# Optimization experiments

Hardware: AMD Instinct MI355X
Metric: run time of the kernel (lower is better)

Reference implementation:

```python
import jax, jax.numpy as jnp
import numpy as np

N_HEAD = 16

def _proj(W, b, x):
    # 1x1 Conv2d: x is (b, e, h, w) -> (b, o, h, w)
    return jnp.einsum('oe,behw->bohw', W, x) + b[None, :, None, None]

def setup_inputs() -> dict:
    key = jax.random.key(0)
    ks = jax.random.split(key, 12)
    B, E, S = 2, 1024, 2048
    d_qk, d_v, d_out = E, E, E
    def xavier(k, o, i):
        bound = np.sqrt(6.0 / (o + i))
        return jax.random.uniform(k, (o, i), jnp.float32, -bound, bound)
    return {
        'q': jax.random.normal(ks[0], (B, E, 1, S), jnp.float32),
        'k': jax.random.normal(ks[1], (B, E, 1, S), jnp.float32),
        'v': jax.random.normal(ks[2], (B, E, 1, S), jnp.float32),
        'qk_mask': jax.random.normal(ks[3], (B, S, 1, S), jnp.float32),
        'Wq': xavier(ks[4], d_qk, E), 'bq': jnp.zeros((d_qk,), jnp.float32),
        'Wk': xavier(ks[5], d_qk, E), 'bk': jnp.zeros((d_qk,), jnp.float32),
        'Wv': xavier(ks[6], d_v, E), 'bv': jnp.zeros((d_v,), jnp.float32),
        'Wo': xavier(ks[7], d_out, d_v), 'bo': jnp.zeros((d_out,), jnp.float32),
    }

def reference(q, k, v, qk_mask, Wq, bq, Wk, bk, Wv, bv, Wo, bo):
    # q,k,v: (B, E, 1, S); qk_mask: (B, S_src, 1, S_tgt)
    qp = _proj(Wq, bq, q)
    kp = _proj(Wk, bk, k)
    vp = _proj(Wv, bv, v)
    B, C, _, S = qp.shape
    H = N_HEAD
    dh = C // H
    scale = float(dh) ** -0.5
    qh = (qp * scale).reshape(B, H, dh, S)   # (b, h, c, q)
    kh = kp.reshape(B, H, dh, S)             # (b, h, c, k)
    vh = vp.reshape(B, H, dh, S)             # (b, h, c, k)
    # per-head scores, equivalent to the split einsum 'bchq,bkhc->bkhq'
    scores = jnp.einsum('bhcq,bhck->bhkq', qh, kh)        # (b, h, k, q)
    scores = scores + qk_mask[:, None, :, 0, :]           # mask broadcast over heads
    w = jax.nn.softmax(scores, axis=2)                    # softmax over key dim (dim=1 per-head)
    attn = jnp.einsum('bhkq,bhck->bhcq', w, vh).reshape(B, C, 1, S)
    return _proj(Wo, bo, attn)
```

## Files before the change

kernel.cpp:

```cpp
#include <hip/hip_runtime.h>
#include <hip/hip_bf16.h>

typedef unsigned short ushort_t;
typedef __attribute__((ext_vector_type(8))) __bf16 bf16x8;
typedef __attribute__((ext_vector_type(4))) float f32x4;
typedef __attribute__((ext_vector_type(2))) unsigned int u32x2;
typedef __attribute__((ext_vector_type(8))) unsigned short us8;

#define DEV __device__ __forceinline__

constexpr int BB = 2, EE = 1024, SS = 2048, HH = 16;
constexpr float L2E = 1.44269504088896f;
constexpr float SCALE_Q = 0.125f * 1.44269504088896f;

DEV ushort_t f2bf(float x) {
  union { float f; unsigned u; } c; c.f = x;
  unsigned u = c.u;
  return (ushort_t)((u + 0x7fffu + ((u >> 16) & 1u)) >> 16);
}

DEV unsigned cvtpk(float lo, float hi) {
  unsigned r;
  asm volatile("v_cvt_pk_bf16_f32 %0, %1, %2" : "=v"(r) : "v"(lo), "v"(hi));
  return r;
}

DEV void gload16(const void* g, void* l) {
  __builtin_amdgcn_global_load_lds((const __attribute__((address_space(1))) void*)g,
                                   (__attribute__((address_space(3))) void*)l, 16, 0, 0);
}

struct TpArgs { const float* i0; const float* i1; const float* i2;
                ushort_t* o0; ushort_t* o1; ushort_t* o2; };

__global__ __launch_bounds__(256) void k_transpose_cvt(TpArgs a) {
  int z = blockIdx.z; int p = z >> 1; int b = z & 1;
  const float* in = (p == 0) ? a.i0 : (p == 1) ? a.i1 : a.i2;
  ushort_t* out = (p == 0) ? a.o0 : (p == 1) ? a.o1 : a.o2;
  in += (long long)b * EE * SS;
  out += (long long)b * SS * EE;
  int s0 = blockIdx.x * 64, e0 = blockIdx.y * 64;
  __shared__ __align__(16) ushort_t T[64][72];
  int t = threadIdx.x;
  int sc = (t & 15) * 4, erb = t >> 4;
#pragma unroll
  for (int it = 0; it < 4; ++it) {
    int er = erb + it * 16;
    float4 v = *(const float4*)(in + (long long)(e0 + er) * SS + s0 + sc);
    T[sc + 0][er] = f2bf(v.x);
    T[sc + 1][er] = f2bf(v.y);
    T[sc + 2][er] = f2bf(v.z);
    T[sc + 3][er] = f2bf(v.w);
  }
  __syncthreads();
#pragma unroll
  for (int it = 0; it < 2; ++it) {
    int slot = t + it * 256;
    int sr = slot >> 3, ec = (slot & 7) * 8;
    us8 v = *(const us8*)&T[sr][ec];
    *(us8*)(out + (long long)(s0 + sr) * EE + e0 + ec) = v;
  }
}

struct WArgs { const float* w0; const float* w1; const float* w2; const float* w3;
               ushort_t* o0; ushort_t* o1; ushort_t* o2; ushort_t* o3; };

__global__ __launch_bounds__(256) void k_cvt_w(WArgs a) {
  int y = blockIdx.y;
  const float* in = (y == 0) ? a.w0 : (y == 1) ? a.w1 : (y == 2) ? a.w2 : a.w3;
  ushort_t* out = (y == 0) ? a.o0 : (y == 1) ? a.o1 : (y == 2) ? a.o2 : a.o3;
  long long idx = ((long long)blockIdx.x * 256 + threadIdx.x) * 4;
  float4 v = *(const float4*)(in + idx);
  unsigned lo = f2bf(v.x) | ((unsigned)f2bf(v.y) << 16);
  unsigned hi = f2bf(v.z) | ((unsigned)f2bf(v.w) << 16);
  u32x2 pk = {lo, hi};
  *(u32x2*)(out + idx) = pk;
}

DEV void stage_tile(const ushort_t* src0, ushort_t* dst0, int w, int lane) {
#pragma unroll
  for (int i = 0; i < 2; ++i) {
    int u = w * 128 + i * 64 + lane;
    int row = u >> 2, part = u & 3;
    gload16(src0 + (long long)row * 1024 + part * 8, dst0 + (w * 128 + i * 64) * 8);
  }
}

__global__ __launch_bounds__(256) void k_proj(
    const ushort_t* __restrict__ xq, const ushort_t* __restrict__ xk,
    const ushort_t* __restrict__ xv, const ushort_t* __restrict__ wq,
    const ushort_t* __restrict__ wk, const ushort_t* __restrict__ wv,
    const float* __restrict__ bqp, const float* __restrict__ bkp,
    const float* __restrict__ bvp,
    ushort_t* __restrict__ qpT, ushort_t* __restrict__ kpT,
    ushort_t* __restrict__ vpN) {
  constexpr int K = 1024;
  __shared__ __align__(16) ushort_t As[2][4096];
  __shared__ __align__(16) ushort_t Bs[2][4096];
  int t = threadIdx.x, lane = t & 63, w = t >> 6;
  int lq = lane & 15, g = lane >> 4;
  int z = blockIdx.z, pair = z >> 1, b = z & 1;
  long long s2 = (long long)SS * EE;
  int m0, n0, LDo; bool browq; float scale; const float* bias;
  const ushort_t *Ab, *Bb; ushort_t* Co;
  if (pair < 2) {
    m0 = blockIdx.y * 128; n0 = blockIdx.x * 128;
    Ab = (pair == 0 ? wq : wk) + (long long)m0 * K;
    Bb = (pair == 0 ? xq : xk) + b * s2 + (long long)n0 * K;
    Co = (pair == 0 ? qpT : kpT) + b * s2;
    bias = (pair == 0 ? bqp : bkp);
    scale = (pair == 0 ? SCALE_Q : 1.0f);
    LDo = EE; browq = true;
  } else {
    m0 = blockIdx.x * 128; n0 = blockIdx.y * 128;
    Ab = xv + b * s2 + (long long)m0 * K;
    Bb = wv + (long long)n0 * K;
    Co = vpN + b * s2;
    bias = bvp; scale = 1.0f; LDo = SS; browq = false;
  }

  f32x4 acc[4][4];
#pragma unroll
  for (int mi = 0; mi < 4; ++mi)
#pragma unroll
    for (int ni = 0; ni < 4; ++ni) acc[mi][ni] = (f32x4){0.f, 0.f, 0.f, 0.f};

  stage_tile(Ab, As[0], w, lane);
  stage_tile(Bb, Bs[0], w, lane);
  __syncthreads();
  int wm = w >> 1, wn = w & 1;
  for (int kt = 0; kt < K / 32; ++kt) {
    int buf = kt & 1;
    if (kt + 1 < K / 32) {
      stage_tile(Ab + (kt + 1) * 32, As[buf ^ 1], w, lane);
      stage_tile(Bb + (kt + 1) * 32, Bs[buf ^ 1], w, lane);
    }
    bf16x8 aF[4], bF[4];
#pragma unroll
    for (int mi = 0; mi < 4; ++mi)
      aF[mi] = *(const bf16x8*)&As[buf][(wm * 64 + mi * 16 + lq) * 32 + g * 8];
#pragma unroll
    for (int ni = 0; ni < 4; ++ni)
      bF[ni] = *(const bf16x8*)&Bs[buf][(wn * 64 + ni * 16 + lq) * 32 + g * 8];
#pragma unroll
    for (int mi = 0; mi < 4; ++mi)
#pragma unroll
      for (int ni = 0; ni < 4; ++ni)
        acc[mi][ni] = __builtin_amdgcn_mfma_f32_16x16x32_bf16(aF[mi], bF[ni], acc[mi][ni], 0, 0, 0);
    __syncthreads();
  }
#pragma unroll
  for (int ni = 0; ni < 4; ++ni) {
    int col = n0 + wn * 64 + ni * 16 + lq;
    float bc = browq ? 0.f : bias[col];
#pragma unroll
    for (int mi = 0; mi < 4; ++mi) {
      int row0 = m0 + wm * 64 + mi * 16 + 4 * g;
      f32x4 v = acc[mi][ni];
#pragma unroll
      for (int r = 0; r < 4; ++r) {
        float bb = browq ? bias[row0 + r] : bc;
        v[r] = (v[r] + bb) * scale;
      }
      u32x2 pk = {cvtpk(v[0], v[1]), cvtpk(v[2], v[3])};
      *(u32x2*)(Co + (long long)col * LDo + row0) = pk;
    }
  }
}

__global__ __launch_bounds__(256) void k_gemm_out(
    const ushort_t* __restrict__ A, long long sA,
    const ushort_t* __restrict__ Bm,
    float* __restrict__ C, long long sC,
    const float* __restrict__ bias, int LDo) {
  constexpr int K = 1024;
  __shared__ __align__(16) ushort_t As[2][4096];
  __shared__ __align__(16) ushort_t Bs[2][4096];
  int t = threadIdx.x, lane = t & 63, w = t >> 6;
  int lq = lane & 15, g = lane >> 4;
  int m0 = blockIdx.y * 128, n0 = blockIdx.x * 128;
  const ushort_t* Ab = A + (long long)blockIdx.z * sA + (long long)m0 * K;
  const ushort_t* Bb = Bm + (long long)n0 * K;

  f32x4 acc[4][4];
#pragma unroll
  for (int mi = 0; mi < 4; ++mi)
#pragma unroll
    for (int ni = 0; ni < 4; ++ni) acc[mi][ni] = (f32x4){0.f, 0.f, 0.f, 0.f};

  stage_tile(Ab, As[0], w, lane);
  stage_tile(Bb, Bs[0], w, lane);
  __syncthreads();
  int wm = w >> 1, wn = w & 1;
  for (int kt = 0; kt < K / 32; ++kt) {
    int buf = kt & 1;
    if (kt + 1 < K / 32) {
      stage_tile(Ab + (kt + 1) * 32, As[buf ^ 1], w, lane);
      stage_tile(Bb + (kt + 1) * 32, Bs[buf ^ 1], w, lane);
    }
    bf16x8 aF[4], bF[4];
#pragma unroll
    for (int mi = 0; mi < 4; ++mi)
      aF[mi] = *(const bf16x8*)&As[buf][(wm * 64 + mi * 16 + lq) * 32 + g * 8];
#pragma unroll
    for (int ni = 0; ni < 4; ++ni)
      bF[ni] = *(const bf16x8*)&Bs[buf][(wn * 64 + ni * 16 + lq) * 32 + g * 8];
#pragma unroll
    for (int mi = 0; mi < 4; ++mi)
#pragma unroll
      for (int ni = 0; ni < 4; ++ni)
        acc[mi][ni] = __builtin_amdgcn_mfma_f32_16x16x32_bf16(aF[mi], bF[ni], acc[mi][ni], 0, 0, 0);
    __syncthreads();
  }
#pragma unroll
  for (int ni = 0; ni < 4; ++ni) {
    int col = n0 + wn * 64 + ni * 16 + lq;
    float bc = bias[col];
#pragma unroll
    for (int mi = 0; mi < 4; ++mi) {
      int row0 = m0 + wm * 64 + mi * 16 + 4 * g;
      f32x4 v = acc[mi][ni];
#pragma unroll
      for (int r = 0; r < 4; ++r) v[r] += bc;
      *(f32x4*)(C + (long long)blockIdx.z * sC + (long long)col * LDo + row0) = v;
    }
  }
}

__global__ __launch_bounds__(256, 4) void k_attn(
    const ushort_t* __restrict__ qpT, const ushort_t* __restrict__ kpT,
    const ushort_t* __restrict__ vp, const float* __restrict__ mask,
    ushort_t* __restrict__ attnT) {
  int t = threadIdx.x, lane = t & 63, w = t >> 6;
  int lq = lane & 15, g = lane >> 4;
  int sw = lq >> 2;
  int kvsw = lq & 7;
  int qt = blockIdx.x, h = blockIdx.y, b = blockIdx.z;
  int q0 = qt * 64;
  long long s2 = (long long)SS * EE;
  const ushort_t* qT = qpT + b * s2;
  const ushort_t* kTb = kpT + b * s2 + h * 64;
  const ushort_t* vB = vp + b * s2 + (long long)(h * 64) * SS;
  const float* mk = mask + (long long)b * SS * SS;
  ushort_t* aT = attnT + b * s2;

  __shared__ __align__(16) ushort_t Kt[2][4096];
  __shared__ __align__(16) ushort_t Vt[2][4096];
  __shared__ __align__(16) ushort_t Pt[4][1024];

  int qglob = q0 + w * 16;
  const float* mbase = mk + qglob + lq;

  bf16x8 qF[2];
#pragma unroll
  for (int ch = 0; ch < 2; ++ch)
    qF[ch] = *(const bf16x8*)(qT + (long long)(qglob + lq) * EE + h * 64 + ch * 32 + g * 8);

  int srow = (lane >> 3);
  int sslot = lane & 7;
  auto stageKV = [&](int buf, int k0) {
#pragma unroll
    for (int i = 0; i < 2; ++i) {
      int row = w * 16 + i * 8 + srow;
      int ps = sslot ^ (row & 7);
      gload16(kTb + (long long)(k0 + row) * EE + ps * 8,
              &Kt[buf][(w * 16 + i * 8) * 64]);
      gload16(vB + (long long)row * SS + k0 + ps * 8,
              &Vt[buf][(w * 16 + i * 8) * 64]);
    }
  };

  stageKV(0, 0);
  __syncthreads();

  f32x4 accO[4];
#pragma unroll
  for (int cf = 0; cf < 4; ++cf) accO[cf] = (f32x4){0.f, 0.f, 0.f, 0.f};
  float mrun = -3e38f, lrun = 0.f;

#pragma unroll 1
  for (int kt = 0; kt < SS / 64; ++kt) {
    int k0 = kt * 64;
    int cur = kt & 1;
    if (kt + 1 < SS / 64) stageKV(cur ^ 1, k0 + 64);

    float mv[4][4];
#pragma unroll
    for (int kf = 0; kf < 4; ++kf)
#pragma unroll
      for (int r = 0; r < 4; ++r)
        mv[kf][r] = mbase[(long long)(k0 + kf * 16 + 4 * g + r) * SS];

    f32x4 accS[4];
#pragma unroll
    for (int kf = 0; kf < 4; ++kf) accS[kf] = (f32x4){0.f, 0.f, 0.f, 0.f};
    __builtin_amdgcn_s_setprio(1);
#pragma unroll
    for (int ch = 0; ch < 2; ++ch) {
      bf16x8 aK[4];
#pragma unroll
      for (int kf = 0; kf < 4; ++kf) {
        int row = kf * 16 + lq;
        aK[kf] = *(const bf16x8*)&Kt[cur][row * 64 + (((ch * 4 + g) ^ kvsw) * 8)];
      }
#pragma unroll
      for (int kf = 0; kf < 4; ++kf)
        accS[kf] = __builtin_amdgcn_mfma_f32_16x16x32_bf16(aK[kf], qF[ch], accS[kf], 0, 0, 0);
    }
    __builtin_amdgcn_s_setprio(0);

    float sv[4][4];
    float tm = -3e38f;
#pragma unroll
    for (int kf = 0; kf < 4; ++kf)
#pragma unroll
      for (int r = 0; r < 4; ++r) {
        sv[kf][r] = fmaf(mv[kf][r], L2E, accS[kf][r]);
        tm = fmaxf(tm, sv[kf][r]);
      }
    tm = fmaxf(tm, __shfl_xor(tm, 16));
    tm = fmaxf(tm, __shfl_xor(tm, 32));
    if (__any(tm > mrun + 8.0f)) {
      float mnew = fmaxf(mrun, tm);
      float corr = __builtin_amdgcn_exp2f(mrun - mnew);
      lrun *= corr;
#pragma unroll
      for (int cf = 0; cf < 4; ++cf) accO[cf] = accO[cf] * corr;
      mrun = mnew;
    }
    float ps = 0.f;
    unsigned pk0[4], pk1[4];
#pragma unroll
    for (int kf = 0; kf < 4; ++kf) {
      float p0 = __builtin_amdgcn_exp2f(sv[kf][0] - mrun);
      float p1 = __builtin_amdgcn_exp2f(sv[kf][1] - mrun);
      float p2 = __builtin_amdgcn_exp2f(sv[kf][2] - mrun);
      float p3 = __builtin_amdgcn_exp2f(sv[kf][3] - mrun);
      ps += (p0 + p1) + (p2 + p3);
      pk0[kf] = cvtpk(p0, p1);
      pk1[kf] = cvtpk(p2, p3);
    }
    ps += __shfl_xor(ps, 16);
    ps += __shfl_xor(ps, 32);
    lrun += ps;
#pragma unroll
    for (int kf = 0; kf < 4; ++kf) {
      int slot = ((kf & 1) * 2 + (g >> 1)) ^ sw;
      u32x2 pkv = {pk0[kf], pk1[kf]};
      *(u32x2*)&Pt[w][(kf >> 1) * 512 + lq * 32 + slot * 8 + (g & 1) * 4] = pkv;
    }

    __builtin_amdgcn_s_setprio(1);
#pragma unroll
    for (int ch = 0; ch < 2; ++ch) {
      bf16x8 bP = *(const bf16x8*)&Pt[w][ch * 512 + lq * 32 + (g ^ sw) * 8];
#pragma unroll
      for (int cf = 0; cf < 4; ++cf) {
        int row = cf * 16 + lq;
        bf16x8 vF = *(const bf16x8*)&Vt[cur][row * 64 + (((ch * 4 + g) ^ kvsw) * 8)];
        accO[cf] = __builtin_amdgcn_mfma_f32_16x16x32_bf16(vF, bP, accO[cf], 0, 0, 0);
      }
    }
    __builtin_amdgcn_s_setprio(0);
    __syncthreads();
  }

  float inv = 1.f / lrun;
  int s = qglob + lq;
#pragma unroll
  for (int cf = 0; cf < 4; ++cf) {
    int c0 = h * 64 + cf * 16 + 4 * g;
    f32x4 v = accO[cf];
    u32x2 pk = {cvtpk(v[0] * inv, v[1] * inv), cvtpk(v[2] * inv, v[3] * inv)};
    *(u32x2*)(aT + (long long)s * EE + c0) = pk;
  }
}

extern "C" void kernel_launch(void* const* d_in, const int* in_sizes, int n_in,
                              void* d_out, int out_size, void* d_ws, size_t ws_size,
                              hipStream_t stream) {
  const float* q = (const float*)d_in[0];
  const float* k = (const float*)d_in[1];
  const float* v = (const float*)d_in[2];
  const float* mask = (const float*)d_in[3];
  const float* Wq = (const float*)d_in[4];
  const float* bq = (const float*)d_in[5];
  const float* Wk = (const float*)d_in[6];
  const float* bk = (const float*)d_in[7];
  const float* Wv = (const float*)d_in[8];
  const float* bv = (const float*)d_in[9];
  const float* Wo = (const float*)d_in[10];
  const float* bo = (const float*)d_in[11];
  float* out = (float*)d_out;

  char* ws = (char*)d_ws;
  const long long MB = 1024LL * 1024LL;
  ushort_t* xqT = (ushort_t*)(ws + 0 * MB);
  ushort_t* xkT = (ushort_t*)(ws + 8 * MB);
  ushort_t* xvT = (ushort_t*)(ws + 16 * MB);
  ushort_t* wqB = (ushort_t*)(ws + 24 * MB);
  ushort_t* wkB = (ushort_t*)(ws + 26 * MB);
  ushort_t* wvB = (ushort_t*)(ws + 28 * MB);
  ushort_t* woB = (ushort_t*)(ws + 30 * MB);
  ushort_t* qpT = (ushort_t*)(ws + 32 * MB);
  ushort_t* kpT = (ushort_t*)(ws + 40 * MB);
  ushort_t* vpN = (ushort_t*)(ws + 48 * MB);
  ushort_t* anT = (ushort_t*)(ws + 56 * MB);

  TpArgs tp{q, k, v, xqT, xkT, xvT};
  hipLaunchKernelGGL(k_transpose_cvt, dim3(SS / 64, EE / 64, 6), dim3(256), 0, stream, tp);
  WArgs wa{Wq, Wk, Wv, Wo, wqB, wkB, wvB, woB};
  hipLaunchKernelGGL(k_cvt_w, dim3(1024, 4, 1), dim3(256), 0, stream, wa);

  hipLaunchKernelGGL(k_proj, dim3(SS / 128, EE / 128, 6), dim3(256), 0, stream,
                     xqT, xkT, xvT, wqB, wkB, wvB, bq, bk, bv, qpT, kpT, vpN);
  hipLaunchKernelGGL(k_attn, dim3(SS / 64, HH, BB), dim3(256), 0, stream,
                     qpT, kpT, vpN, mask, anT);
  long long s2 = (long long)SS * EE;
  hipLaunchKernelGGL(k_gemm_out, dim3(EE / 128, SS / 128, BB), dim3(256), 0, stream,
                     anT, s2, woB, out, s2, bo, SS);
}
```

Measured before the change: 163.9 us.

## Software-pipeline PV matmul of previous tile with QK of current tile

Restructures the attention loop so the P·V MFMAs for the previous key tile run right after the Q·K MFMAs of the current tile. This lets the matrix units overlap with the softmax exp and mask work instead of waiting on it. K and V staging are split, so V for the next tile is prefetched only after the previous V buffer is consumed; this adds a barrier per iteration and a PV epilogue after the loop. The launch bounds also drop the minimum-blocks hint, which may raise register use and lower occupancy.

```diff
diff --git a/kernel.cpp b/kernel.cpp
--- a/kernel.cpp
+++ b/kernel.cpp
@@ -227,7 +227,7 @@
   }
 }
 
-__global__ __launch_bounds__(256, 4) void k_attn(
+__global__ __launch_bounds__(256) void k_attn(
     const ushort_t* __restrict__ qpT, const ushort_t* __restrict__ kpT,
     const ushort_t* __restrict__ vp, const float* __restrict__ mask,
     ushort_t* __restrict__ attnT) {
@@ -258,31 +258,40 @@
 
   int srow = (lane >> 3);
   int sslot = lane & 7;
-  auto stageKV = [&](int buf, int k0) {
+  auto stageK = [&](int buf, int k0) {
 #pragma unroll
     for (int i = 0; i < 2; ++i) {
       int row = w * 16 + i * 8 + srow;
       int ps = sslot ^ (row & 7);
       gload16(kTb + (long long)(k0 + row) * EE + ps * 8,
               &Kt[buf][(w * 16 + i * 8) * 64]);
+    }
+  };
+  auto stageV = [&](int buf, int k0) {
+#pragma unroll
+    for (int i = 0; i < 2; ++i) {
+      int row = w * 16 + i * 8 + srow;
+      int ps = sslot ^ (row & 7);
       gload16(vB + (long long)row * SS + k0 + ps * 8,
               &Vt[buf][(w * 16 + i * 8) * 64]);
     }
   };
 
-  stageKV(0, 0);
+  stageK(0, 0);
+  stageV(0, 0);
   __syncthreads();
 
   f32x4 accO[4];
 #pragma unroll
   for (int cf = 0; cf < 4; ++cf) accO[cf] = (f32x4){0.f, 0.f, 0.f, 0.f};
   float mrun = -3e38f, lrun = 0.f;
+  int cur = 0;
+  constexpr int NT = SS / 64;
 
 #pragma unroll 1
-  for (int kt = 0; kt < SS / 64; ++kt) {
+  for (int kt = 0; kt < NT; ++kt) {
     int k0 = kt * 64;
-    int cur = kt & 1;
-    if (kt + 1 < SS / 64) stageKV(cur ^ 1, k0 + 64);
+    if (kt + 1 < NT) stageK(cur ^ 1, k0 + 64);
 
     float mv[4][4];
 #pragma unroll
@@ -307,7 +316,22 @@
       for (int kf = 0; kf < 4; ++kf)
         accS[kf] = __builtin_amdgcn_mfma_f32_16x16x32_bf16(aK[kf], qF[ch], accS[kf], 0, 0, 0);
     }
+    if (kt) {
+#pragma unroll
+      for (int ch = 0; ch < 2; ++ch) {
+        bf16x8 bP = *(const bf16x8*)&Pt[w][ch * 512 + lq * 32 + (g ^ sw) * 8];
+#pragma unroll
+        for (int cf = 0; cf < 4; ++cf) {
+          int row = cf * 16 + lq;
+          bf16x8 vF = *(const bf16x8*)&Vt[cur ^ 1][row * 64 + (((ch * 4 + g) ^ kvsw) * 8)];
+          accO[cf] = __builtin_amdgcn_mfma_f32_16x16x32_bf16(vF, bP, accO[cf], 0, 0, 0);
+        }
+      }
+    }
     __builtin_amdgcn_s_setprio(0);
+
+    __syncthreads();
+    if (kt + 1 < NT) stageV(cur ^ 1, k0 + 64);
 
     float sv[4][4];
     float tm = -3e38f;
@@ -350,20 +374,22 @@
       *(u32x2*)&Pt[w][(kf >> 1) * 512 + lq * 32 + slot * 8 + (g & 1) * 4] = pkv;
     }
 
-    __builtin_amdgcn_s_setprio(1);
-#pragma unroll
-    for (int ch = 0; ch < 2; ++ch) {
-      bf16x8 bP = *(const bf16x8*)&Pt[w][ch * 512 + lq * 32 + (g ^ sw) * 8];
-#pragma unroll
-      for (int cf = 0; cf < 4; ++cf) {
-        int row = cf * 16 + lq;
-        bf16x8 vF = *(const bf16x8*)&Vt[cur][row * 64 + (((ch * 4 + g) ^ kvsw) * 8)];
-        accO[cf] = __builtin_amdgcn_mfma_f32_16x16x32_bf16(vF, bP, accO[cf], 0, 0, 0);
-      }
-    }
-    __builtin_amdgcn_s_setprio(0);
     __syncthreads();
-  }
+    cur ^= 1;
+  }
+
+  __builtin_amdgcn_s_setprio(1);
+#pragma unroll
+  for (int ch = 0; ch < 2; ++ch) {
+    bf16x8 bP = *(const bf16x8*)&Pt[w][ch * 512 + lq * 32 + (g ^ sw) * 8];
+#pragma unroll
+    for (int cf = 0; cf < 4; ++cf) {
+      int row = cf * 16 + lq;
+      bf16x8 vF = *(const bf16x8*)&Vt[cur ^ 1][row * 64 + (((ch * 4 + g) ^ kvsw) * 8)];
+      accO[cf] = __builtin_amdgcn_mfma_f32_16x16x32_bf16(vF, bP, accO[cf], 0, 0, 0);
+    }
+  }
+  __builtin_amdgcn_s_setprio(0);
 
   float inv = 1.f / lrun;
   int s = qglob + lq;
```

New measurement: 170.7 us. 1.04x slower.
